# Optimization experiments

Hardware: AMD Instinct MI355X
Metric: run time of the kernel (lower is better)

The kernel has to match this reference:

```python
import jax, jax.numpy as jnp
import numpy as np

WS = 15
PAD = WS // 2
BN_EPS = 1e-5


def _unfold2d(a, ws):
    # a: (b, t, c, H, W) already padded -> (b, t, c, h, w, ws, ws), stride-1 windows
    h = a.shape[3] - ws + 1
    w = a.shape[4] - ws + 1
    ih = (jnp.arange(h)[:, None] + jnp.arange(ws)[None, :])  # (h, ws)
    iw = (jnp.arange(w)[:, None] + jnp.arange(ws)[None, :])  # (w, ws)
    return a[:, :, :, ih[:, None, :, None], iw[None, :, None, :]]


def setup_inputs() -> dict:
    key = jax.random.key(0)
    ks = jax.random.split(key, 11)
    b, t_mem, c, h, w = 2, 2, 256, 32, 32
    s = 0.05
    return {
        "x": jax.random.normal(ks[0], (b, c, h, w), jnp.float32),
        "mem": jax.random.normal(ks[1], (b, t_mem, c, h, w), jnp.float32),
        "w_qk": jax.random.normal(ks[2], (c // 8, c), jnp.float32) * s,
        "w_qv": jax.random.normal(ks[3], (c // 2, c), jnp.float32) * s,
        "w_mk": jax.random.normal(ks[4], (c // 8, c), jnp.float32) * s,
        "w_mv": jax.random.normal(ks[5], (c // 2, c), jnp.float32) * s,
        "w_smooth": jax.random.normal(ks[6], (c, c), jnp.float32) * s,
        "bn_gamma": jax.random.uniform(ks[7], (c,), jnp.float32, 0.5, 1.5),
        "bn_beta": jax.random.normal(ks[8], (c,), jnp.float32) * 0.1,
        "bn_mean": jnp.zeros((c,), jnp.float32),
        "bn_var": jnp.ones((c,), jnp.float32),
    }


def reference(x, mem, w_qk, w_qv, w_mk, w_mv, w_smooth, bn_gamma, bn_beta, bn_mean, bn_var):
    # mem <- cat([x, mem]) along time: (b, t, c, h, w)
    mem = jnp.concatenate([x[:, None], mem], axis=1)
    b, t, c, h, w = mem.shape

    # 1x1 convs == per-pixel matmuls
    query_k = jnp.einsum('bchw,oc->bohw', x, w_qk)          # (b, c/8, h, w)
    query_v = jnp.einsum('bchw,oc->bohw', x, w_qv)          # (b, c/2, h, w); Dropout2d(p=0) is identity
    mem_k = jnp.einsum('btchw,oc->btohw', mem, w_mk)        # (b, t, c/8, h, w)
    mem_v = jnp.einsum('btchw,oc->btohw', mem, w_mv)        # (b, t, c/2, h, w)

    pad = [(0, 0), (0, 0), (0, 0), (PAD, PAD), (PAD, PAD)]
    unf_k = _unfold2d(jnp.pad(mem_k, pad), WS)              # (b, t, c/8, h, w, ws, ws)
    unf_v = _unfold2d(jnp.pad(mem_v, pad), WS)              # (b, t, c/2, h, w, ws, ws)

    attn = jnp.einsum('bchw,btchwxy->bhwtxy', query_k, unf_k)
    attn = attn.reshape(b, h, w, t * WS * WS)
    # NOTE: faithful to original: softmax over dim=2 (the spatial w axis), not over keys
    attn = jax.nn.softmax(attn, axis=2)

    unf_v = jnp.transpose(unf_v, (0, 2, 3, 4, 1, 5, 6)).reshape(b, c // 2, h, w, t * WS * WS)
    mem_out = jnp.einsum('bhwk,bchwk->bchw', attn, unf_v)   # (b, c/2, h, w)

    feat = jnp.concatenate([query_v, mem_out], axis=1)      # (b, c, h, w)
    y = jnp.einsum('bchw,oc->bohw', feat, w_smooth)
    # BatchNorm2d in eval mode (running stats) + ReLU
    inv = bn_gamma / jnp.sqrt(bn_var + BN_EPS)
    y = y * inv[None, :, None, None] + (bn_beta - bn_mean * inv)[None, :, None, None]
    return jax.nn.relu(y)
```

## Files before the change

kernel.cpp:

```cpp
#include <hip/hip_runtime.h>
#include <math.h>

#define HWSZ 1024
#define HH 32
#define WW 32
#define C 256
#define CK 32
#define CV 128
#define T 3
#define WSZ 15
#define PADSZ 7
#define PADDED 46
#define PP (PADDED*PADDED)
#define KK (T*WSZ*WSZ)
#define B 2
#define NOUT 160
#define KC 32
#define PIXT 32

static const size_t OFF_QK   = 0;
static const size_t OFF_QV   = 65536;
static const size_t OFF_MK   = 327680;
static const size_t OFF_MV   = 733952;
static const size_t OFF_ATTN = 2359040;
static const size_t OFF_PART = 3741440;
static const size_t ZERO_N   = 406272 + 1625088;

__global__ __launch_bounds__(256) void k_zero(float* __restrict__ p, int n) {
    int i = blockIdx.x * 256 + threadIdx.x;
    if (i < n) p[i] = 0.f;
}

__global__ __launch_bounds__(256) void k_proj(
    const float* __restrict__ x, const float* __restrict__ mem,
    const float* __restrict__ w_qk, const float* __restrict__ w_qv,
    const float* __restrict__ w_mk, const float* __restrict__ w_mv,
    float* __restrict__ ws)
{
    __shared__ float inT[KC][PIXT];
    __shared__ float wT[NOUT][KC + 1];

    int jb   = blockIdx.x >> 5;
    int rowt = blockIdx.x & 31;
    int tid  = threadIdx.x;
    int tx   = tid & 7;
    int ty   = tid >> 3;

    int b, t;
    const float *wk, *wv;
    bool isq;
    if (jb < 6) { b = jb / 3; t = jb % 3; wk = w_mk; wv = w_mv; isq = false; }
    else        { b = jb - 6; t = 0;      wk = w_qk; wv = w_qv; isq = true;  }

    const float* src = (t == 0)
        ? (x + ((size_t)b * C) * HWSZ)
        : (mem + ((size_t)(b * (T - 1) + (t - 1)) * C) * HWSZ);
    int hw0 = rowt * WW;

    float acc[5][4];
    #pragma unroll
    for (int j = 0; j < 5; j++)
        #pragma unroll
        for (int i = 0; i < 4; i++) acc[j][i] = 0.f;

    for (int c0 = 0; c0 < C; c0 += KC) {
        {
            int cc = tid >> 3;
            int p4 = (tid & 7) * 4;
            float4 v = *(const float4*)&src[(size_t)(c0 + cc) * HWSZ + hw0 + p4];
            inT[cc][p4 + 0] = v.x; inT[cc][p4 + 1] = v.y;
            inT[cc][p4 + 2] = v.z; inT[cc][p4 + 3] = v.w;
        }
        #pragma unroll
        for (int j = 0; j < 5; j++) {
            int f  = tid + j * 256;
            int o  = f >> 3;
            int c4 = (f & 7) * 4;
            const float* wr = (o < CK) ? (wk + (size_t)o * C) : (wv + (size_t)(o - CK) * C);
            float4 v = *(const float4*)&wr[c0 + c4];
            wT[o][c4 + 0] = v.x; wT[o][c4 + 1] = v.y;
            wT[o][c4 + 2] = v.z; wT[o][c4 + 3] = v.w;
        }
        __syncthreads();

        #pragma unroll 8
        for (int k = 0; k < KC; k++) {
            float4 iv = *(const float4*)&inT[k][tx * 4];
            #pragma unroll
            for (int j = 0; j < 5; j++) {
                float wv_ = wT[ty * 5 + j][k];
                acc[j][0] += wv_ * iv.x; acc[j][1] += wv_ * iv.y;
                acc[j][2] += wv_ * iv.z; acc[j][3] += wv_ * iv.w;
            }
        }
        __syncthreads();
    }

    int hq = rowt, yp = hq + PADSZ;
    float* mk = ws + OFF_MK;
    float* mv = ws + OFF_MV;
    #pragma unroll
    for (int j = 0; j < 5; j++) {
        int o = ty * 5 + j;
        #pragma unroll
        for (int i = 0; i < 4; i++) {
            int wq = tx * 4 + i;
            float v = acc[j][i];
            if (!isq) {
                int xp = wq + PADSZ;
                if (o < CK)
                    mk[(((size_t)(b * T + t) * CK + o) * PP) + yp * PADDED + xp] = v;
                else
                    mv[((size_t)(b * T + t) * PP + yp * PADDED + xp) * CV + (o - CK)] = v;
            } else {
                int hw = hq * WW + wq;
                if (o < CK) ws[OFF_QK + ((size_t)b * HWSZ + hw) * CK + o] = v;
                else        ws[OFF_QV + ((size_t)(b * CV + (o - CK))) * HWSZ + hw] = v;
            }
        }
    }
}

__global__ __launch_bounds__(256) void k_attn_sm(
    const float* __restrict__ qk, const float* __restrict__ mk,
    float* __restrict__ attn)
{
    __shared__ float mkl[PADDED][36];
    __shared__ float ql[WW][36];

    int blk = blockIdx.x;
    int xx  = blk % WSZ;
    int rem = blk / WSZ;
    int t   = rem % T;
    int bh  = rem / T;
    int b   = bh >> 5, hq = bh & 31;
    int tid = threadIdx.x;
    int w   = tid & 31;
    int ty  = tid >> 5;

    const float* mkb = mk + ((size_t)(b * T + t) * CK) * PP;

    for (int f = tid; f < PADDED * CK; f += 256) {
        int c = f / PADDED, col = f - c * PADDED;
        mkl[col][c] = mkb[(size_t)c * PP + (size_t)(hq + xx) * PADDED + col];
    }
    for (int f = tid; f < WW * CK; f += 256) {
        int w2 = f >> 5, c = f & 31;
        ql[w2][c] = qk[((size_t)(b * HWSZ + hq * WW + w2)) * CK + c];
    }
    __syncthreads();

    float4 q[8];
    #pragma unroll
    for (int i = 0; i < 8; i++) q[i] = *(const float4*)&ql[w][i * 4];

    int yy0 = ty;
    int yy1 = ty + 8;
    int row1 = (yy1 < WSZ) ? yy1 : 14;

    float s0 = 0.f, s1 = 0.f;
    #pragma unroll
    for (int cq = 0; cq < 8; cq++) {
        float4 m0 = *(const float4*)&mkl[w + yy0][cq * 4];
        float4 m1 = *(const float4*)&mkl[w + row1][cq * 4];
        s0 += q[cq].x * m0.x + q[cq].y * m0.y + q[cq].z * m0.z + q[cq].w * m0.w;
        s1 += q[cq].x * m1.x + q[cq].y * m1.y + q[cq].z * m1.z + q[cq].w * m1.w;
    }

    float m0 = s0, m1 = s1;
    #pragma unroll
    for (int d = 1; d < 32; d <<= 1) {
        m0 = fmaxf(m0, __shfl_xor(m0, d, 32));
        m1 = fmaxf(m1, __shfl_xor(m1, d, 32));
    }
    float e0 = __expf(s0 - m0), e1 = __expf(s1 - m1);
    float t0 = e0, t1 = e1;
    #pragma unroll
    for (int d = 1; d < 32; d <<= 1) {
        t0 += __shfl_xor(t0, d, 32);
        t1 += __shfl_xor(t1, d, 32);
    }
    float a0 = e0 / t0, a1 = e1 / t1;

    float* aout = attn + ((size_t)bh * KK + t * WSZ * WSZ + xx * WSZ) * WW;
    aout[yy0 * WW + w] = a0;
    if (yy1 < WSZ) aout[yy1 * WW + w] = a1;
}

__global__ __launch_bounds__(256) void k_av(
    const float* __restrict__ attn, const float* __restrict__ mv,
    float* __restrict__ part)
{
    __shared__ float V[PADDED][132];
    __shared__ float al[WSZ * WW];

    int blk = blockIdx.x;
    int xg  = blk % 3;
    int rem = blk / 3;
    int t   = rem % T;
    int bh  = rem / T;
    int b   = bh >> 5, hq = bh & 31;
    int tid = threadIdx.x;
    int wq  = tid & 7;
    int cg  = tid >> 3;
    int w0  = wq * 4;
    int c0  = cg * 4;

    const float* mvb = mv + (size_t)(b * T + t) * PP * CV;
    const float* ab  = attn + ((size_t)bh * KK + t * WSZ * WSZ) * WW;

    float acc[4][4];
    #pragma unroll
    for (int ci = 0; ci < 4; ci++)
        #pragma unroll
        for (int wi = 0; wi < 4; wi++) acc[ci][wi] = 0.f;

    for (int xi = 0; xi < 5; xi++) {
        int xx = xg * 5 + xi;
        for (int f = tid; f < PADDED * 32; f += 256) {
            int col = f >> 5, cq = f & 31;
            float4 v4 = *(const float4*)&mvb[((size_t)(hq + xx) * PADDED + col) * CV + cq * 4];
            V[col][cq * 4 + 0] = v4.x; V[col][cq * 4 + 1] = v4.y;
            V[col][cq * 4 + 2] = v4.z; V[col][cq * 4 + 3] = v4.w;
        }
        for (int f = tid; f < WSZ * WW; f += 256)
            al[f] = ab[(size_t)(xx * WSZ) * WW + f];
        __syncthreads();

        float4 vw[18];
        #pragma unroll
        for (int i = 0; i < 18; i++)
            vw[i] = *(const float4*)&V[w0 + i][c0];

        #pragma unroll
        for (int yy = 0; yy < WSZ; yy++) {
            float4 a4 = *(const float4*)&al[yy * WW + w0];
            #pragma unroll
            for (int wi = 0; wi < 4; wi++) {
                float av = (wi == 0) ? a4.x : (wi == 1) ? a4.y : (wi == 2) ? a4.z : a4.w;
                float4 vv = vw[yy + wi];
                acc[0][wi] += av * vv.x;
                acc[1][wi] += av * vv.y;
                acc[2][wi] += av * vv.z;
                acc[3][wi] += av * vv.w;
            }
        }
        __syncthreads();
    }

    float* pbase = part + ((size_t)(bh * 9 + (t * 3 + xg)) * CV) * WW;
    #pragma unroll
    for (int ci = 0; ci < 4; ci++) {
        float4 r; r.x = acc[ci][0]; r.y = acc[ci][1]; r.z = acc[ci][2]; r.w = acc[ci][3];
        *(float4*)&pbase[(c0 + ci) * WW + w0] = r;
    }
}

__global__ __launch_bounds__(256) void k_out(
    const float* __restrict__ qv, const float* __restrict__ part,
    const float* __restrict__ wsm,
    const float* __restrict__ g, const float* __restrict__ bta,
    const float* __restrict__ mean, const float* __restrict__ var,
    float* __restrict__ out)
{
    __shared__ float inT[KC][PIXT];
    __shared__ float wTt[KC][132];

    int blk  = blockIdx.x;
    int oh   = blk & 1;
    int rowt = (blk >> 1) & 31;
    int b    = blk >> 6;
    int tid  = threadIdx.x;
    int tx   = tid & 7;
    int ty   = tid >> 3;
    int hw0  = rowt * WW;
    int obase = oh * 128;
    int bh   = b * HH + rowt;

    float acc[4][4];
    #pragma unroll
    for (int j = 0; j < 4; j++)
        #pragma unroll
        for (int i = 0; i < 4; i++) acc[j][i] = 0.f;

    for (int c0 = 0; c0 < C; c0 += KC) {
        {
            int cc = tid >> 3;
            int p4 = (tid & 7) * 4;
            float4 v;
            if (c0 < CV) {
                v = *(const float4*)&qv[((size_t)(b * CV + c0 + cc)) * HWSZ + hw0 + p4];
            } else {
                int cloc = (c0 - CV) + cc;
                const float* pb = part + ((size_t)bh * 9) * CV * WW + cloc * WW + p4;
                float4 s = *(const float4*)pb;
                #pragma unroll
                for (int tg = 1; tg < 9; tg++) {
                    float4 a = *(const float4*)&pb[(size_t)tg * CV * WW];
                    s.x += a.x; s.y += a.y; s.z += a.z; s.w += a.w;
                }
                v = s;
            }
            inT[cc][p4 + 0] = v.x; inT[cc][p4 + 1] = v.y;
            inT[cc][p4 + 2] = v.z; inT[cc][p4 + 3] = v.w;
        }
        #pragma unroll
        for (int j = 0; j < 4; j++) {
            int f  = tid + j * 256;
            int o  = f >> 3;
            int c4 = (f & 7) * 4;
            float4 v = *(const float4*)&wsm[(size_t)(obase + o) * C + c0 + c4];
            wTt[c4 + 0][o] = v.x; wTt[c4 + 1][o] = v.y;
            wTt[c4 + 2][o] = v.z; wTt[c4 + 3][o] = v.w;
        }
        __syncthreads();

        #pragma unroll 8
        for (int k = 0; k < KC; k++) {
            float4 iv  = *(const float4*)&inT[k][tx * 4];
            float4 wv4 = *(const float4*)&wTt[k][ty * 4];
            acc[0][0] += wv4.x * iv.x; acc[0][1] += wv4.x * iv.y;
            acc[0][2] += wv4.x * iv.z; acc[0][3] += wv4.x * iv.w;
            acc[1][0] += wv4.y * iv.x; acc[1][1] += wv4.y * iv.y;
            acc[1][2] += wv4.y * iv.z; acc[1][3] += wv4.y * iv.w;
            acc[2][0] += wv4.z * iv.x; acc[2][1] += wv4.z * iv.y;
            acc[2][2] += wv4.z * iv.z; acc[2][3] += wv4.z * iv.w;
            acc[3][0] += wv4.w * iv.x; acc[3][1] += wv4.w * iv.y;
            acc[3][2] += wv4.w * iv.z; acc[3][3] += wv4.w * iv.w;
        }
        __syncthreads();
    }

    #pragma unroll
    for (int j = 0; j < 4; j++) {
        int o = obase + ty * 4 + j;
        float inv = g[o] * rsqrtf(var[o] + 1e-5f);
        float sh  = bta[o] - mean[o] * inv;
        float4 r;
        r.x = fmaxf(acc[j][0] * inv + sh, 0.f);
        r.y = fmaxf(acc[j][1] * inv + sh, 0.f);
        r.z = fmaxf(acc[j][2] * inv + sh, 0.f);
        r.w = fmaxf(acc[j][3] * inv + sh, 0.f);
        *(float4*)&out[((size_t)(b * C + o)) * HWSZ + hw0 + tx * 4] = r;
    }
}

extern "C" void kernel_launch(void* const* d_in, const int* in_sizes, int n_in,
                              void* d_out, int out_size, void* d_ws, size_t ws_size,
                              hipStream_t stream) {
    const float* x    = (const float*)d_in[0];
    const float* mem  = (const float*)d_in[1];
    const float* w_qk = (const float*)d_in[2];
    const float* w_qv = (const float*)d_in[3];
    const float* w_mk = (const float*)d_in[4];
    const float* w_mv = (const float*)d_in[5];
    const float* wsm  = (const float*)d_in[6];
    const float* g    = (const float*)d_in[7];
    const float* bta  = (const float*)d_in[8];
    const float* mean = (const float*)d_in[9];
    const float* var  = (const float*)d_in[10];
    float* out = (float*)d_out;
    float* ws  = (float*)d_ws;

    {
        int n = (int)ZERO_N;
        k_zero<<<(n + 255) / 256, 256, 0, stream>>>(ws + OFF_MK, n);
    }
    k_proj<<<8 * 32, 256, 0, stream>>>(x, mem, w_qk, w_qv, w_mk, w_mv, ws);
    k_attn_sm<<<B * HH * T * WSZ, 256, 0, stream>>>(ws + OFF_QK, ws + OFF_MK, ws + OFF_ATTN);
    k_av<<<B * HH * T * 3, 256, 0, stream>>>(ws + OFF_ATTN, ws + OFF_MV, ws + OFF_PART);
    k_out<<<B * 32 * 2, 256, 0, stream>>>(ws + OFF_QV, ws + OFF_PART, wsm, g, bta, mean, var, out);
}
```

Measured before the change: 86.59 us.

## Fuse attention softmax with AV, accumulate via atomics, fold zeroing into projection

Merges the attention-score and AV kernels into one kernel, so the attention weights stay in shared memory instead of going through global memory. Each block atomically adds its partial output into a pre-zeroed mem_out buffer, which replaces the 9-way partial-sum reduction in the output kernel. The separate zero kernel is removed: the projection kernel now zeroes only the pad borders and the mem_out buffer. This saves two launches and the attention and partial-sum round-trips, at the cost of many float atomics and a V tile that is reloaded per block rather than reused across 5 window rows.

```diff
diff --git a/kernel.cpp b/kernel.cpp
--- a/kernel.cpp
+++ b/kernel.cpp
@@ -18,18 +18,11 @@
 #define KC 32
 #define PIXT 32
 
-static const size_t OFF_QK   = 0;
-static const size_t OFF_QV   = 65536;
-static const size_t OFF_MK   = 327680;
-static const size_t OFF_MV   = 733952;
-static const size_t OFF_ATTN = 2359040;
-static const size_t OFF_PART = 3741440;
-static const size_t ZERO_N   = 406272 + 1625088;
-
-__global__ __launch_bounds__(256) void k_zero(float* __restrict__ p, int n) {
-    int i = blockIdx.x * 256 + threadIdx.x;
-    if (i < n) p[i] = 0.f;
-}
+static const size_t OFF_QK = 0;
+static const size_t OFF_QV = 65536;
+static const size_t OFF_MK = 327680;
+static const size_t OFF_MV = 733952;
+static const size_t OFF_MO = 2359040;
 
 __global__ __launch_bounds__(256) void k_proj(
     const float* __restrict__ x, const float* __restrict__ mem,
@@ -57,6 +50,46 @@
         : (mem + ((size_t)(b * (T - 1) + (t - 1)) * C) * HWSZ);
     int hw0 = rowt * WW;
 
+    float* mk = ws + OFF_MK;
+    float* mv = ws + OFF_MV;
+    float* mo = ws + OFF_MO;
+    size_t bt = (size_t)(b * T + t);
+
+    if (!isq) {
+        int yp = rowt + PADSZ;
+        for (int f = tid; f < 448 + 1792; f += 256) {
+            if (f < 448) {
+                int c = f / 14, sc = f % 14;
+                int col = (sc < 7) ? sc : sc + 25;
+                mk[(bt * CK + c) * PP + yp * PADDED + col] = 0.f;
+            } else {
+                int g = f - 448;
+                int sc = g >> 7, c = g & 127;
+                int col = (sc < 7) ? sc : sc + 25;
+                mv[(bt * PP + yp * PADDED + col) * CV + c] = 0.f;
+            }
+        }
+        if (rowt < 14) {
+            int pr = (rowt < 7) ? rowt : rowt + 32;
+            for (int f = tid; f < 1472 + 5888; f += 256) {
+                if (f < 1472) {
+                    int c = f / PADDED, col = f % PADDED;
+                    mk[(bt * CK + c) * PP + pr * PADDED + col] = 0.f;
+                } else {
+                    int g = f - 1472;
+                    int col = g >> 7, c = g & 127;
+                    mv[(bt * PP + pr * PADDED + col) * CV + c] = 0.f;
+                }
+            }
+        }
+    } else {
+        int qi = (jb - 6) * 32 + rowt;
+        float4 z; z.x = z.y = z.z = z.w = 0.f;
+        float* base = mo + (size_t)qi * 4096;
+        for (int f = tid; f < 1024; f += 256)
+            *(float4*)&base[f * 4] = z;
+    }
+
     float acc[5][4];
     #pragma unroll
     for (int j = 0; j < 5; j++)
@@ -97,8 +130,6 @@
     }
 
     int hq = rowt, yp = hq + PADSZ;
-    float* mk = ws + OFF_MK;
-    float* mv = ws + OFF_MV;
     #pragma unroll
     for (int j = 0; j < 5; j++) {
         int o = ty * 5 + j;
@@ -109,9 +140,9 @@
             if (!isq) {
                 int xp = wq + PADSZ;
                 if (o < CK)
-                    mk[(((size_t)(b * T + t) * CK + o) * PP) + yp * PADDED + xp] = v;
+                    mk[(bt * CK + o) * PP + yp * PADDED + xp] = v;
                 else
-                    mv[((size_t)(b * T + t) * PP + yp * PADDED + xp) * CV + (o - CK)] = v;
+                    mv[(bt * PP + yp * PADDED + xp) * CV + (o - CK)] = v;
             } else {
                 int hw = hq * WW + wq;
                 if (o < CK) ws[OFF_QK + ((size_t)b * HWSZ + hw) * CK + o] = v;
@@ -121,12 +152,14 @@
     }
 }
 
-__global__ __launch_bounds__(256) void k_attn_sm(
+__global__ __launch_bounds__(256) void k_attn_av(
     const float* __restrict__ qk, const float* __restrict__ mk,
-    float* __restrict__ attn)
+    const float* __restrict__ mv, float* __restrict__ mo)
 {
     __shared__ float mkl[PADDED][36];
     __shared__ float ql[WW][36];
+    __shared__ float V[PADDED][132];
+    __shared__ float al[WSZ][WW];
 
     int blk = blockIdx.x;
     int xx  = blk % WSZ;
@@ -135,11 +168,16 @@
     int bh  = rem / T;
     int b   = bh >> 5, hq = bh & 31;
     int tid = threadIdx.x;
-    int w   = tid & 31;
-    int ty  = tid >> 5;
 
     const float* mkb = mk + ((size_t)(b * T + t) * CK) * PP;
-
+    const float* mvb = mv + (size_t)(b * T + t) * PP * CV;
+
+    for (int f = tid; f < PADDED * 32; f += 256) {
+        int col = f >> 5, cq = f & 31;
+        float4 v4 = *(const float4*)&mvb[((size_t)(hq + xx) * PADDED + col) * CV + cq * 4];
+        V[col][cq * 4 + 0] = v4.x; V[col][cq * 4 + 1] = v4.y;
+        V[col][cq * 4 + 2] = v4.z; V[col][cq * 4 + 3] = v4.w;
+    }
     for (int f = tid; f < PADDED * CK; f += 256) {
         int c = f / PADDED, col = f - c * PADDED;
         mkl[col][c] = mkb[(size_t)c * PP + (size_t)(hq + xx) * PADDED + col];
@@ -150,91 +188,61 @@
     }
     __syncthreads();
 
-    float4 q[8];
-    #pragma unroll
-    for (int i = 0; i < 8; i++) q[i] = *(const float4*)&ql[w][i * 4];
-
-    int yy0 = ty;
-    int yy1 = ty + 8;
-    int row1 = (yy1 < WSZ) ? yy1 : 14;
-
-    float s0 = 0.f, s1 = 0.f;
-    #pragma unroll
-    for (int cq = 0; cq < 8; cq++) {
-        float4 m0 = *(const float4*)&mkl[w + yy0][cq * 4];
-        float4 m1 = *(const float4*)&mkl[w + row1][cq * 4];
-        s0 += q[cq].x * m0.x + q[cq].y * m0.y + q[cq].z * m0.z + q[cq].w * m0.w;
-        s1 += q[cq].x * m1.x + q[cq].y * m1.y + q[cq].z * m1.z + q[cq].w * m1.w;
-    }
-
-    float m0 = s0, m1 = s1;
-    #pragma unroll
-    for (int d = 1; d < 32; d <<= 1) {
-        m0 = fmaxf(m0, __shfl_xor(m0, d, 32));
-        m1 = fmaxf(m1, __shfl_xor(m1, d, 32));
-    }
-    float e0 = __expf(s0 - m0), e1 = __expf(s1 - m1);
-    float t0 = e0, t1 = e1;
-    #pragma unroll
-    for (int d = 1; d < 32; d <<= 1) {
-        t0 += __shfl_xor(t0, d, 32);
-        t1 += __shfl_xor(t1, d, 32);
-    }
-    float a0 = e0 / t0, a1 = e1 / t1;
-
-    float* aout = attn + ((size_t)bh * KK + t * WSZ * WSZ + xx * WSZ) * WW;
-    aout[yy0 * WW + w] = a0;
-    if (yy1 < WSZ) aout[yy1 * WW + w] = a1;
-}
-
-__global__ __launch_bounds__(256) void k_av(
-    const float* __restrict__ attn, const float* __restrict__ mv,
-    float* __restrict__ part)
-{
-    __shared__ float V[PADDED][132];
-    __shared__ float al[WSZ * WW];
-
-    int blk = blockIdx.x;
-    int xg  = blk % 3;
-    int rem = blk / 3;
-    int t   = rem % T;
-    int bh  = rem / T;
-    int b   = bh >> 5, hq = bh & 31;
-    int tid = threadIdx.x;
-    int wq  = tid & 7;
-    int cg  = tid >> 3;
-    int w0  = wq * 4;
-    int c0  = cg * 4;
-
-    const float* mvb = mv + (size_t)(b * T + t) * PP * CV;
-    const float* ab  = attn + ((size_t)bh * KK + t * WSZ * WSZ) * WW;
-
-    float acc[4][4];
-    #pragma unroll
-    for (int ci = 0; ci < 4; ci++)
-        #pragma unroll
-        for (int wi = 0; wi < 4; wi++) acc[ci][wi] = 0.f;
-
-    for (int xi = 0; xi < 5; xi++) {
-        int xx = xg * 5 + xi;
-        for (int f = tid; f < PADDED * 32; f += 256) {
-            int col = f >> 5, cq = f & 31;
-            float4 v4 = *(const float4*)&mvb[((size_t)(hq + xx) * PADDED + col) * CV + cq * 4];
-            V[col][cq * 4 + 0] = v4.x; V[col][cq * 4 + 1] = v4.y;
-            V[col][cq * 4 + 2] = v4.z; V[col][cq * 4 + 3] = v4.w;
-        }
-        for (int f = tid; f < WSZ * WW; f += 256)
-            al[f] = ab[(size_t)(xx * WSZ) * WW + f];
-        __syncthreads();
+    {
+        int w  = tid & 31;
+        int ty = tid >> 5;
+        float4 q[8];
+        #pragma unroll
+        for (int i = 0; i < 8; i++) q[i] = *(const float4*)&ql[w][i * 4];
+
+        int yy0 = ty, yy1 = ty + 8;
+        int row1 = (yy1 < WSZ) ? yy1 : 14;
+
+        float s0 = 0.f, s1 = 0.f;
+        #pragma unroll
+        for (int cq = 0; cq < 8; cq++) {
+            float4 m0 = *(const float4*)&mkl[w + yy0][cq * 4];
+            float4 m1 = *(const float4*)&mkl[w + row1][cq * 4];
+            s0 += q[cq].x * m0.x + q[cq].y * m0.y + q[cq].z * m0.z + q[cq].w * m0.w;
+            s1 += q[cq].x * m1.x + q[cq].y * m1.y + q[cq].z * m1.z + q[cq].w * m1.w;
+        }
+
+        float m0 = s0, m1 = s1;
+        #pragma unroll
+        for (int d = 1; d < 32; d <<= 1) {
+            m0 = fmaxf(m0, __shfl_xor(m0, d, 32));
+            m1 = fmaxf(m1, __shfl_xor(m1, d, 32));
+        }
+        float e0 = __expf(s0 - m0), e1 = __expf(s1 - m1);
+        float t0 = e0, t1 = e1;
+        #pragma unroll
+        for (int d = 1; d < 32; d <<= 1) {
+            t0 += __shfl_xor(t0, d, 32);
+            t1 += __shfl_xor(t1, d, 32);
+        }
+        al[yy0][w] = e0 / t0;
+        if (yy1 < WSZ) al[yy1][w] = e1 / t1;
+    }
+    __syncthreads();
+
+    {
+        int wq = tid & 7, cg = tid >> 3;
+        int w0 = wq * 4, c0 = cg * 4;
 
         float4 vw[18];
         #pragma unroll
         for (int i = 0; i < 18; i++)
             vw[i] = *(const float4*)&V[w0 + i][c0];
 
+        float acc[4][4];
+        #pragma unroll
+        for (int ci = 0; ci < 4; ci++)
+            #pragma unroll
+            for (int wi = 0; wi < 4; wi++) acc[ci][wi] = 0.f;
+
         #pragma unroll
         for (int yy = 0; yy < WSZ; yy++) {
-            float4 a4 = *(const float4*)&al[yy * WW + w0];
+            float4 a4 = *(const float4*)&al[yy][w0];
             #pragma unroll
             for (int wi = 0; wi < 4; wi++) {
                 float av = (wi == 0) ? a4.x : (wi == 1) ? a4.y : (wi == 2) ? a4.z : a4.w;
@@ -245,19 +253,18 @@
                 acc[3][wi] += av * vv.w;
             }
         }
-        __syncthreads();
-    }
-
-    float* pbase = part + ((size_t)(bh * 9 + (t * 3 + xg)) * CV) * WW;
-    #pragma unroll
-    for (int ci = 0; ci < 4; ci++) {
-        float4 r; r.x = acc[ci][0]; r.y = acc[ci][1]; r.z = acc[ci][2]; r.w = acc[ci][3];
-        *(float4*)&pbase[(c0 + ci) * WW + w0] = r;
+
+        float* mob = mo + ((size_t)b * CV) * HWSZ + hq * WW;
+        #pragma unroll
+        for (int ci = 0; ci < 4; ci++)
+            #pragma unroll
+            for (int wi = 0; wi < 4; wi++)
+                atomicAdd(&mob[(size_t)(c0 + ci) * HWSZ + w0 + wi], acc[ci][wi]);
     }
 }
 
 __global__ __launch_bounds__(256) void k_out(
-    const float* __restrict__ qv, const float* __restrict__ part,
+    const float* __restrict__ qv, const float* __restrict__ mo,
     const float* __restrict__ wsm,
     const float* __restrict__ g, const float* __restrict__ bta,
     const float* __restrict__ mean, const float* __restrict__ var,
@@ -275,7 +282,6 @@
     int ty   = tid >> 3;
     int hw0  = rowt * WW;
     int obase = oh * 128;
-    int bh   = b * HH + rowt;
 
     float acc[4][4];
     #pragma unroll
@@ -287,20 +293,9 @@
         {
             int cc = tid >> 3;
             int p4 = (tid & 7) * 4;
-            float4 v;
-            if (c0 < CV) {
-                v = *(const float4*)&qv[((size_t)(b * CV + c0 + cc)) * HWSZ + hw0 + p4];
-            } else {
-                int cloc = (c0 - CV) + cc;
-                const float* pb = part + ((size_t)bh * 9) * CV * WW + cloc * WW + p4;
-                float4 s = *(const float4*)pb;
-                #pragma unroll
-                for (int tg = 1; tg < 9; tg++) {
-                    float4 a = *(const float4*)&pb[(size_t)tg * CV * WW];
-                    s.x += a.x; s.y += a.y; s.z += a.z; s.w += a.w;
-                }
-                v = s;
-            }
+            const float* srcbuf = (c0 < CV) ? qv : mo;
+            int cb = (c0 < CV) ? c0 : c0 - CV;
+            float4 v = *(const float4*)&srcbuf[((size_t)(b * CV + cb + cc)) * HWSZ + hw0 + p4];
             inT[cc][p4 + 0] = v.x; inT[cc][p4 + 1] = v.y;
             inT[cc][p4 + 2] = v.z; inT[cc][p4 + 3] = v.w;
         }
@@ -362,12 +357,9 @@
     float* out = (float*)d_out;
     float* ws  = (float*)d_ws;
 
-    {
-        int n = (int)ZERO_N;
-        k_zero<<<(n + 255) / 256, 256, 0, stream>>>(ws + OFF_MK, n);
-    }
     k_proj<<<8 * 32, 256, 0, stream>>>(x, mem, w_qk, w_qv, w_mk, w_mv, ws);
-    k_attn_sm<<<B * HH * T * WSZ, 256, 0, stream>>>(ws + OFF_QK, ws + OFF_MK, ws + OFF_ATTN);
-    k_av<<<B * HH * T * 3, 256, 0, stream>>>(ws + OFF_ATTN, ws + OFF_MV, ws + OFF_PART);
-    k_out<<<B * 32 * 2, 256, 0, stream>>>(ws + OFF_QV, ws + OFF_PART, wsm, g, bta, mean, var, out);
+    k_attn_av<<<B * HH * T * WSZ, 256, 0, stream>>>(ws + OFF_QK, ws + OFF_MK,
+                                                    ws + OFF_MV, ws + OFF_MO);
+    k_out<<<B * 32 * 2, 256, 0, stream>>>(ws + OFF_QV, ws + OFF_MO, wsm,
+                                          g, bta, mean, var, out);
 }
```

Result: slower. 222.4 us (+156.9%).
